# Performance work log

Measured on AMD Instinct MI355X. Metric: run time of the kernel, lower is better.

Reference implementation:

```python
import jax, jax.numpy as jnp
import numpy as np

B, C, D, H, W = 4, 256, 16, 16, 16
INTER = C // 8  # 32


def setup_inputs() -> dict:
    key = jax.random.key(0)
    ks = jax.random.split(key, 8)
    return {
        "x": jax.random.normal(ks[0], (B, C, D, H, W), dtype=jnp.float32),
        "Wq": jax.random.normal(ks[1], (INTER, C), dtype=jnp.float32) * 0.05,
        "bq": jax.random.normal(ks[2], (INTER,), dtype=jnp.float32) * 0.05,
        "Wk": jax.random.normal(ks[3], (INTER, C), dtype=jnp.float32) * 0.05,
        "bk": jax.random.normal(ks[4], (INTER,), dtype=jnp.float32) * 0.05,
        "Wv": jax.random.normal(ks[5], (C, C), dtype=jnp.float32) * 0.05,
        "bv": jax.random.normal(ks[6], (C,), dtype=jnp.float32) * 0.05,
        "gamma": jax.random.normal(ks[7], (1,), dtype=jnp.float32),
    }


def reference(x, Wq, bq, Wk, bk, Wv, bv, gamma):
    b, c, d, h, w = x.shape
    n = d * h * w
    xf = x.reshape(b, c, n)  # [B, C, N]
    # 1x1 Conv3d == pointwise channel projection
    q = jnp.einsum("oc,bcn->bon", Wq, xf) + bq[None, :, None]  # [B, inter, N]
    k = jnp.einsum("oc,bcn->bon", Wk, xf) + bk[None, :, None]  # [B, inter, N]
    v = jnp.einsum("oc,bcn->bon", Wv, xf) + bv[None, :, None]  # [B, C, N]
    scale = float(q.shape[1]) ** 0.5
    # attn[b, i, j] = <q[:, i], k[:, j]>
    attn = jax.nn.softmax(jnp.einsum("bci,bcj->bij", q, k) / scale, axis=-1)
    # out[b, c, i] = sum_j v[b, c, j] * attn[b, i, j]
    out = jnp.einsum("bcj,bij->bci", v, attn).reshape(b, c, d, h, w)
    return gamma[0] * out + x
```

## Files before the change

### kernel.cpp

```cpp
#include <hip/hip_runtime.h>

#define B_ 4
#define C_ 256
#define N_ 4096
#define INTER_ 32

typedef __attribute__((ext_vector_type(8))) short short8;
typedef __attribute__((ext_vector_type(4))) float f32x4;
typedef __attribute__((ext_vector_type(16))) float f32x16;
typedef __attribute__((ext_vector_type(4))) unsigned int u32x4;

#define TILEB 18432
#define NSTG  (8 * TILEB)

static __device__ __forceinline__ unsigned short f2bf(float f) {
    unsigned int u = __builtin_bit_cast(unsigned int, f);
    u += 0x7fff + ((u >> 16) & 1);
    return (unsigned short)(u >> 16);
}

static __device__ __forceinline__ unsigned int cvtpk(float lo, float hi) {
    unsigned int r;
    asm("v_cvt_pk_bf16_f32 %0, %1, %2" : "=v"(r) : "v"(lo), "v"(hi));
    return r;
}

static __device__ __forceinline__ void pl32swap(unsigned int& a, unsigned int& b) {
    asm("v_permlane32_swap_b32 %0, %1" : "+v"(a), "+v"(b));
}

static __device__ __forceinline__ void gload16(const void* g, void* l) {
    __builtin_amdgcn_global_load_lds(
        (const __attribute__((address_space(1))) void*)g,
        (__attribute__((address_space(3))) void*)l, 16, 0, 0);
}

__global__ __launch_bounds__(256) void prep_kernel(
    const float* __restrict__ Wq, const float* __restrict__ Wk,
    const float* __restrict__ Wv, unsigned short* __restrict__ wb)
{
    int i = blockIdx.x * 256 + threadIdx.x;
    int row = i >> 8, col = i & 255;
    float v;
    if (row < 32)      v = Wq[row * 256 + col];
    else if (row < 64) v = Wk[(row - 32) * 256 + col];
    else               v = Wv[(row - 64) * 256 + col];
    wb[i] = f2bf(v);
}

__global__ __launch_bounds__(256) void qkv_kernel(
    const float* __restrict__ x, const unsigned short* __restrict__ wb,
    const float* __restrict__ bq, const float* __restrict__ bk,
    const float* __restrict__ bv,
    unsigned short* __restrict__ qb, unsigned short* __restrict__ kfrag,
    unsigned short* __restrict__ vfrag)
{
    const int tid  = threadIdx.x;
    const int wave = tid >> 6;
    const int lane = tid & 63;
    const int l31  = lane & 31;
    const int h2   = lane >> 5;
    const int b    = blockIdx.x >> 6;
    const int n0   = (blockIdx.x & 63) * 64;

    __shared__ unsigned int xsh[64 * 129];

    {
        const float* xb = x + ((size_t)b * C_ + 64 * wave) * N_ + n0 + lane;
        unsigned int* dst = xsh + (size_t)lane * 129 + 32 * wave;
        #pragma unroll 8
        for (int s = 0; s < 32; ++s) {
            float v0 = xb[(size_t)(2 * s) * N_];
            float v1 = xb[(size_t)(2 * s + 1) * N_];
            dst[s] = (unsigned int)f2bf(v0) | ((unsigned int)f2bf(v1) << 16);
        }
    }
    __syncthreads();

    const float rs = 0.17677669529663687f;

    #pragma unroll
    for (int u = 0; u < 5; ++u) {
        const int unit = wave + 4 * u;
        const int ch = unit >> 1;
        const int ns = unit & 1;
        const int ncol = n0 + 32 * ns + l31;
        const int jt = (n0 >> 5) + ns;

        const float* bias = (ch == 0) ? bq : (ch == 1) ? bk : (bv + (ch - 2) * 32);
        f32x16 acc;
        #pragma unroll
        for (int r = 0; r < 16; ++r)
            acc[r] = bias[(r & 3) + 8 * (r >> 2) + 4 * h2];

        const unsigned short* wrow = wb + ((size_t)(ch * 32 + l31)) * 256 + 8 * h2;
        const unsigned int*   xrow = xsh + (size_t)(32 * ns + l31) * 129 + 4 * h2;

        #pragma unroll
        for (int kk = 0; kk < 16; ++kk) {
            short8 wa = *reinterpret_cast<const short8*>(wrow + 16 * kk);
            short8 xf = *reinterpret_cast<const short8*>(xrow + 8 * kk);
            acc = __builtin_amdgcn_mfma_f32_32x32x16_bf16(wa, xf, acc, 0, 0, 0);
        }

        if (ch == 0) {
            unsigned short* dst = qb + ((size_t)b * N_ + ncol) * 32;
            #pragma unroll
            for (int q = 0; q < 4; ++q) {
                unsigned int w0 = (unsigned int)f2bf(acc[4 * q] * rs)
                                | ((unsigned int)f2bf(acc[4 * q + 1] * rs) << 16);
                unsigned int w1 = (unsigned int)f2bf(acc[4 * q + 2] * rs)
                                | ((unsigned int)f2bf(acc[4 * q + 3] * rs) << 16);
                unsigned int* p = reinterpret_cast<unsigned int*>(dst + 4 * h2 + 8 * q);
                p[0] = w0; p[1] = w1;
            }
        } else if (ch == 1) {
            unsigned short* kt = kfrag + ((size_t)b * 128 + jt) * 1024;
            #pragma unroll
            for (int r = 0; r < 16; ++r) {
                const int co = (r & 3) + 8 * (r >> 2) + 4 * h2;
                const int addr = ((co >> 4) << 9) + ((l31 + 32 * ((co >> 3) & 1)) << 3)
                               + (co & 7);
                kt[addr] = f2bf(acc[r]);
            }
        } else {
            const int g = ch - 2;
            unsigned short* vt_ = vfrag + (((size_t)b * 128 + jt) * 8 + g) * 1024;
            #pragma unroll
            for (int r = 0; r < 16; ++r) {
                const int co = (r & 3) + 8 * (r >> 2) + 4 * h2;
                const int addr = ((l31 >> 4) << 9) + ((co + 32 * ((l31 >> 3) & 1)) << 3)
                               + (l31 & 7);
                vt_[addr] = f2bf(acc[r]);
            }
        }
    }
}

__global__ __launch_bounds__(512) void attn_kernel(
    const unsigned short* __restrict__ qb, const unsigned short* __restrict__ kfrag,
    const unsigned short* __restrict__ vfrag,
    const float* __restrict__ x, const float* __restrict__ gamma,
    float* __restrict__ out)
{
    const int tid  = threadIdx.x;
    const int wave = tid >> 6;
    const int lane = tid & 63;
    const int l31  = lane & 31;
    const int h2   = lane >> 5;
    const int jq   = wave >> 1;
    const int qs   = wave & 1;
    const int b    = blockIdx.y;
    const int iq   = blockIdx.x * 64 + 32 * qs;

    __shared__ char lds[NSTG];
    __shared__ float m_sh[8][32];
    __shared__ float l_sh[8][32];

    const unsigned short* vtb = vfrag + (size_t)b * 128 * 8192;
    const unsigned short* ktb = kfrag + (size_t)b * 128 * 1024;

    char* reg0 = lds + (jq * 2) * TILEB;
    char* reg1 = reg0 + TILEB;

    short8 qf0 = *reinterpret_cast<const short8*>(
        qb + ((size_t)b * N_ + iq + l31) * 32 + 8 * h2);
    short8 qf1 = *reinterpret_cast<const short8*>(
        qb + ((size_t)b * N_ + iq + l31) * 32 + 8 * h2 + 16);

    f32x16 acc[8];
    #pragma unroll
    for (int g = 0; g < 8; ++g)
        #pragma unroll
        for (int r = 0; r < 16; ++r) acc[g][r] = 0.f;

    float m_run = 0.f;
    float l_run = 0.f;
    const f32x16 z16 = {};

    {
        const char* vs = (const char*)(vtb + (size_t)(jq * 32) * 8192);
        const char* ks = (const char*)(ktb + (size_t)(jq * 32) * 1024);
        #pragma unroll
        for (int s2 = 0; s2 < 9; ++s2) {
            const int off = qs * 9216 + s2 * 1024;
            const char* g = (off < 16384) ? (vs + off) : (ks + (off - 16384));
            gload16(g + lane * 16, reg0 + off);
        }
    }
    __syncthreads();

    #pragma unroll 1
    for (int t = 0; t < 32; ++t) {
        char* cur = (t & 1) ? reg1 : reg0;
        char* nxt = (t & 1) ? reg0 : reg1;

        if (t < 31) {
            const int jtg = jq * 32 + t + 1;
            const char* vs = (const char*)(vtb + (size_t)jtg * 8192);
            const char* ks = (const char*)(ktb + (size_t)jtg * 1024);
            #pragma unroll
            for (int s2 = 0; s2 < 9; ++s2) {
                const int off = qs * 9216 + s2 * 1024;
                const char* g = (off < 16384) ? (vs + off) : (ks + (off - 16384));
                gload16(g + lane * 16, nxt + off);
            }
        }

        const char* kt_ = cur + 16384;
        short8 ka0 = *reinterpret_cast<const short8*>(kt_ + lane * 16);
        short8 ka1 = *reinterpret_cast<const short8*>(kt_ + 1024 + lane * 16);
        f32x16 s = __builtin_amdgcn_mfma_f32_32x32x16_bf16(ka0, qf0, z16, 0, 0, 0);
        s = __builtin_amdgcn_mfma_f32_32x32x16_bf16(ka1, qf1, s, 0, 0, 0);

        float a0 = fmaxf(s[0], s[8]),  a1 = fmaxf(s[1], s[9]);
        float a2 = fmaxf(s[2], s[10]), a3 = fmaxf(s[3], s[11]);
        float a4 = fmaxf(s[4], s[12]), a5 = fmaxf(s[5], s[13]);
        float a6 = fmaxf(s[6], s[14]), a7 = fmaxf(s[7], s[15]);
        a0 = fmaxf(a0, a4); a1 = fmaxf(a1, a5); a2 = fmaxf(a2, a6); a3 = fmaxf(a3, a7);
        float smax = fmaxf(fmaxf(a0, a1), fmaxf(a2, a3));

        if (__any(smax > m_run + 5.5f)) {
            float sm2 = fmaxf(smax, __shfl_xor(smax, 32));
            float mnew = fmaxf(m_run, sm2);
            float corr = __expf(m_run - mnew);
            m_run = mnew;
            l_run *= corr;
            #pragma unroll
            for (int g = 0; g < 8; ++g)
                #pragma unroll
                for (int r = 0; r < 16; ++r) acc[g][r] *= corr;
        }

        float p[16];
        float lsum = 0.f;
        #pragma unroll
        for (int r = 0; r < 16; ++r) { p[r] = __expf(s[r] - m_run); lsum += p[r]; }
        l_run += lsum;

        unsigned int X0 = cvtpk(p[0],  p[1]),  X1 = cvtpk(p[2],  p[3]);
        unsigned int Y0 = cvtpk(p[4],  p[5]),  Y1 = cvtpk(p[6],  p[7]);
        unsigned int W0 = cvtpk(p[8],  p[9]),  W1 = cvtpk(p[10], p[11]);
        unsigned int V0 = cvtpk(p[12], p[13]), V1 = cvtpk(p[14], p[15]);
        pl32swap(X0, Y0); pl32swap(X1, Y1);
        pl32swap(W0, V0); pl32swap(W1, V1);
        short8 pb0 = __builtin_bit_cast(short8, u32x4{X0, X1, Y0, Y1});
        short8 pb1 = __builtin_bit_cast(short8, u32x4{W0, W1, V0, V1});

        __builtin_amdgcn_s_setprio(1);
        #pragma unroll
        for (int g = 0; g < 8; ++g) {
            short8 va0 = *reinterpret_cast<const short8*>(cur + g * 2048 + lane * 16);
            short8 va1 = *reinterpret_cast<const short8*>(cur + g * 2048 + 1024 + lane * 16);
            acc[g] = __builtin_amdgcn_mfma_f32_32x32x16_bf16(va0, pb0, acc[g], 0, 0, 0);
            acc[g] = __builtin_amdgcn_mfma_f32_32x32x16_bf16(va1, pb1, acc[g], 0, 0, 0);
        }
        __builtin_amdgcn_s_setprio(0);

        __syncthreads();
    }

    float l_tot = l_run + __shfl_xor(l_run, 32);
    if (lane < 32) { m_sh[wave][lane] = m_run; l_sh[wave][lane] = l_tot; }
    __syncthreads();

    float M = -1e30f, L = 0.f;
    #pragma unroll
    for (int w2 = 0; w2 < 4; ++w2) M = fmaxf(M, m_sh[w2 * 2 + qs][l31]);
    #pragma unroll
    for (int w2 = 0; w2 < 4; ++w2)
        L += __expf(m_sh[w2 * 2 + qs][l31] - M) * l_sh[w2 * 2 + qs][l31];
    const float wgt = __expf(m_run - M);
    #pragma unroll
    for (int g = 0; g < 8; ++g)
        #pragma unroll
        for (int r = 0; r < 16; ++r) acc[g][r] *= wgt;

    if (jq >= 2) {
        f32x4* Dr = (f32x4*)(lds + ((jq - 2) * 2 + qs) * 32768);
        #pragma unroll
        for (int g = 0; g < 8; ++g)
            #pragma unroll
            for (int r4 = 0; r4 < 4; ++r4) {
                f32x4 tv;
                #pragma unroll
                for (int e = 0; e < 4; ++e) tv[e] = acc[g][4 * r4 + e];
                Dr[(g * 4 + r4) * 64 + lane] = tv;
            }
    }
    __syncthreads();
    if (jq < 2) {
        const f32x4* Dr = (const f32x4*)(lds + (jq * 2 + qs) * 32768);
        #pragma unroll
        for (int g = 0; g < 8; ++g)
            #pragma unroll
            for (int r4 = 0; r4 < 4; ++r4) {
                f32x4 tv = Dr[(g * 4 + r4) * 64 + lane];
                #pragma unroll
                for (int e = 0; e < 4; ++e) acc[g][4 * r4 + e] += tv[e];
            }
    }
    __syncthreads();
    if (jq == 1) {
        f32x4* Dr = (f32x4*)(lds + (2 + qs) * 32768);
        #pragma unroll
        for (int g = 0; g < 8; ++g)
            #pragma unroll
            for (int r4 = 0; r4 < 4; ++r4) {
                f32x4 tv;
                #pragma unroll
                for (int e = 0; e < 4; ++e) tv[e] = acc[g][4 * r4 + e];
                Dr[(g * 4 + r4) * 64 + lane] = tv;
            }
    }
    __syncthreads();
    if (jq == 0) {
        const f32x4* Dr = (const f32x4*)(lds + (2 + qs) * 32768);
        f32x4* Dw = (f32x4*)(lds + qs * 32768);
        #pragma unroll
        for (int g = 0; g < 8; ++g)
            #pragma unroll
            for (int r4 = 0; r4 < 4; ++r4) {
                f32x4 tv = Dr[(g * 4 + r4) * 64 + lane];
                #pragma unroll
                for (int e = 0; e < 4; ++e) tv[e] += acc[g][4 * r4 + e];
                Dw[(g * 4 + r4) * 64 + lane] = tv;
            }
    }
    __syncthreads();

    const float gma  = gamma[0];
    const float invL = 1.f / L;
    const f32x4* Ds = (const f32x4*)(lds + qs * 32768);
    const int i = iq + l31;
    #pragma unroll
    for (int gi = 0; gi < 2; ++gi) {
        const int g = jq * 2 + gi;
        #pragma unroll
        for (int r4 = 0; r4 < 4; ++r4) {
            f32x4 v = Ds[(g * 4 + r4) * 64 + lane];
            #pragma unroll
            for (int e = 0; e < 4; ++e) {
                const int c = 32 * g + e + 8 * r4 + 4 * h2;
                const size_t off = ((size_t)b * C_ + c) * N_ + i;
                out[off] = gma * v[e] * invL + x[off];
            }
        }
    }
}

extern "C" void kernel_launch(void* const* d_in, const int* in_sizes, int n_in,
                              void* d_out, int out_size, void* d_ws, size_t ws_size,
                              hipStream_t stream) {
    const float* x     = (const float*)d_in[0];
    const float* Wq    = (const float*)d_in[1];
    const float* bq    = (const float*)d_in[2];
    const float* Wk    = (const float*)d_in[3];
    const float* bk    = (const float*)d_in[4];
    const float* Wv    = (const float*)d_in[5];
    const float* bv    = (const float*)d_in[6];
    const float* gamma = (const float*)d_in[7];
    float* out = (float*)d_out;

    unsigned short* ws = (unsigned short*)d_ws;
    unsigned short* qb    = ws;
    unsigned short* kfrag = qb + (size_t)B_ * N_ * INTER_;
    unsigned short* vfrag = kfrag + (size_t)B_ * 128 * 1024;
    unsigned short* wb    = vfrag + (size_t)B_ * 128 * 8192;

    prep_kernel<<<dim3(320), 256, 0, stream>>>(Wq, Wk, Wv, wb);
    qkv_kernel<<<dim3(B_ * (N_ / 64)), 256, 0, stream>>>(
        x, wb, bq, bk, bv, qb, kfrag, vfrag);
    attn_kernel<<<dim3(N_ / 64, B_), 512, 0, stream>>>(
        qb, kfrag, vfrag, x, gamma, out);
}
```

Measured before the change: 84.60 us.

## Process two query tiles per wave, drop per-iteration block barriers, use exp2 softmax

The attention kernel now runs 4 waves per block, and each wave handles both 32-query halves of the 64-query tile. Each K/V tile loaded into LDS is therefore reused for two sets of MFMAs. Each wave streams its own K/V range into a private double buffer, which removes the per-iteration __syncthreads. The q scale is folded with log2(e) so the softmax can use exp2f, and the rescale threshold is raised. Blocks are remapped so each XCD works on one batch for L2 locality. The cost is higher register pressure from two accumulator sets, plus a serialized two-pass LDS reduction at the end.

Result: slower. 197.0 us (+132.9%).

```diff
diff --git a/kernel.cpp b/kernel.cpp
--- a/kernel.cpp
+++ b/kernel.cpp
@@ -11,7 +11,6 @@
 typedef __attribute__((ext_vector_type(4))) unsigned int u32x4;
 
 #define TILEB 18432
-#define NSTG  (8 * TILEB)
 
 static __device__ __forceinline__ unsigned short f2bf(float f) {
     unsigned int u = __builtin_bit_cast(unsigned int, f);
@@ -77,7 +76,7 @@
     }
     __syncthreads();
 
-    const float rs = 0.17677669529663687f;
+    const float rs = 0.25504183f;
 
     #pragma unroll
     for (int u = 0; u < 5; ++u) {
@@ -137,7 +136,7 @@
     }
 }
 
-__global__ __launch_bounds__(512) void attn_kernel(
+__global__ __launch_bounds__(256, 1) void attn_kernel(
     const unsigned short* __restrict__ qb, const unsigned short* __restrict__ kfrag,
     const unsigned short* __restrict__ vfrag,
     const float* __restrict__ x, const float* __restrict__ gamma,
@@ -148,202 +147,219 @@
     const int lane = tid & 63;
     const int l31  = lane & 31;
     const int h2   = lane >> 5;
-    const int jq   = wave >> 1;
-    const int qs   = wave & 1;
-    const int b    = blockIdx.y;
-    const int iq   = blockIdx.x * 64 + 32 * qs;
-
-    __shared__ char lds[NSTG];
-    __shared__ float m_sh[8][32];
-    __shared__ float l_sh[8][32];
+
+    const int bid  = blockIdx.x;
+    const int xcd  = bid & 7;
+    const int slot = bid >> 3;
+    const int b    = xcd >> 1;
+    const int ib   = slot * 2 + (xcd & 1);
+    const int i0   = ib * 64;
+
+    __shared__ char lds[4 * 2 * TILEB];
+    __shared__ float m_sh[4][2][32];
+    __shared__ float l_sh[4][2][32];
 
     const unsigned short* vtb = vfrag + (size_t)b * 128 * 8192;
     const unsigned short* ktb = kfrag + (size_t)b * 128 * 1024;
 
-    char* reg0 = lds + (jq * 2) * TILEB;
-    char* reg1 = reg0 + TILEB;
-
-    short8 qf0 = *reinterpret_cast<const short8*>(
-        qb + ((size_t)b * N_ + iq + l31) * 32 + 8 * h2);
-    short8 qf1 = *reinterpret_cast<const short8*>(
-        qb + ((size_t)b * N_ + iq + l31) * 32 + 8 * h2 + 16);
-
-    f32x16 acc[8];
+    char* buf0 = lds + wave * (2 * TILEB);
+    char* buf1 = buf0 + TILEB;
+
+#define STAGE(jtg_, dst_) do {                                                \
+        const char* vs_ = (const char*)(vtb + (size_t)(jtg_) * 8192);         \
+        _Pragma("unroll")                                                     \
+        for (int s2_ = 0; s2_ < 16; ++s2_)                                    \
+            gload16(vs_ + s2_ * 1024 + lane * 16, (dst_) + s2_ * 1024);       \
+        const char* ks_ = (const char*)(ktb + (size_t)(jtg_) * 1024);         \
+        gload16(ks_ + lane * 16, (dst_) + 16384);                             \
+        gload16(ks_ + 1024 + lane * 16, (dst_) + 17408);                      \
+    } while (0)
+
+    const unsigned short* qbase = qb + ((size_t)b * N_ + i0 + l31) * 32 + 8 * h2;
+    short8 qa0 = *reinterpret_cast<const short8*>(qbase);
+    short8 qa1 = *reinterpret_cast<const short8*>(qbase + 16);
+    short8 qb0 = *reinterpret_cast<const short8*>(qbase + 32 * 32);
+    short8 qb1 = *reinterpret_cast<const short8*>(qbase + 32 * 32 + 16);
+
+    f32x16 accA[8], accB[8];
     #pragma unroll
     for (int g = 0; g < 8; ++g)
         #pragma unroll
-        for (int r = 0; r < 16; ++r) acc[g][r] = 0.f;
-
-    float m_run = 0.f;
-    float l_run = 0.f;
+        for (int r = 0; r < 16; ++r) { accA[g][r] = 0.f; accB[g][r] = 0.f; }
+
+    float mA = 0.f, lA = 0.f, mB = 0.f, lB = 0.f;
     const f32x16 z16 = {};
 
-    {
-        const char* vs = (const char*)(vtb + (size_t)(jq * 32) * 8192);
-        const char* ks = (const char*)(ktb + (size_t)(jq * 32) * 1024);
-        #pragma unroll
-        for (int s2 = 0; s2 < 9; ++s2) {
-            const int off = qs * 9216 + s2 * 1024;
-            const char* g = (off < 16384) ? (vs + off) : (ks + (off - 16384));
-            gload16(g + lane * 16, reg0 + off);
-        }
-    }
-    __syncthreads();
+    STAGE(wave * 32, buf0);
+    asm volatile("s_waitcnt vmcnt(0)" ::: "memory");
+    __builtin_amdgcn_sched_barrier(0);
 
     #pragma unroll 1
     for (int t = 0; t < 32; ++t) {
-        char* cur = (t & 1) ? reg1 : reg0;
-        char* nxt = (t & 1) ? reg0 : reg1;
-
-        if (t < 31) {
-            const int jtg = jq * 32 + t + 1;
-            const char* vs = (const char*)(vtb + (size_t)jtg * 8192);
-            const char* ks = (const char*)(ktb + (size_t)jtg * 1024);
-            #pragma unroll
-            for (int s2 = 0; s2 < 9; ++s2) {
-                const int off = qs * 9216 + s2 * 1024;
-                const char* g = (off < 16384) ? (vs + off) : (ks + (off - 16384));
-                gload16(g + lane * 16, nxt + off);
-            }
-        }
-
-        const char* kt_ = cur + 16384;
-        short8 ka0 = *reinterpret_cast<const short8*>(kt_ + lane * 16);
-        short8 ka1 = *reinterpret_cast<const short8*>(kt_ + 1024 + lane * 16);
-        f32x16 s = __builtin_amdgcn_mfma_f32_32x32x16_bf16(ka0, qf0, z16, 0, 0, 0);
-        s = __builtin_amdgcn_mfma_f32_32x32x16_bf16(ka1, qf1, s, 0, 0, 0);
-
-        float a0 = fmaxf(s[0], s[8]),  a1 = fmaxf(s[1], s[9]);
-        float a2 = fmaxf(s[2], s[10]), a3 = fmaxf(s[3], s[11]);
-        float a4 = fmaxf(s[4], s[12]), a5 = fmaxf(s[5], s[13]);
-        float a6 = fmaxf(s[6], s[14]), a7 = fmaxf(s[7], s[15]);
-        a0 = fmaxf(a0, a4); a1 = fmaxf(a1, a5); a2 = fmaxf(a2, a6); a3 = fmaxf(a3, a7);
-        float smax = fmaxf(fmaxf(a0, a1), fmaxf(a2, a3));
-
-        if (__any(smax > m_run + 5.5f)) {
-            float sm2 = fmaxf(smax, __shfl_xor(smax, 32));
-            float mnew = fmaxf(m_run, sm2);
-            float corr = __expf(m_run - mnew);
-            m_run = mnew;
-            l_run *= corr;
-            #pragma unroll
-            for (int g = 0; g < 8; ++g)
-                #pragma unroll
-                for (int r = 0; r < 16; ++r) acc[g][r] *= corr;
-        }
-
-        float p[16];
-        float lsum = 0.f;
-        #pragma unroll
-        for (int r = 0; r < 16; ++r) { p[r] = __expf(s[r] - m_run); lsum += p[r]; }
-        l_run += lsum;
-
-        unsigned int X0 = cvtpk(p[0],  p[1]),  X1 = cvtpk(p[2],  p[3]);
-        unsigned int Y0 = cvtpk(p[4],  p[5]),  Y1 = cvtpk(p[6],  p[7]);
-        unsigned int W0 = cvtpk(p[8],  p[9]),  W1 = cvtpk(p[10], p[11]);
-        unsigned int V0 = cvtpk(p[12], p[13]), V1 = cvtpk(p[14], p[15]);
-        pl32swap(X0, Y0); pl32swap(X1, Y1);
-        pl32swap(W0, V0); pl32swap(W1, V1);
-        short8 pb0 = __builtin_bit_cast(short8, u32x4{X0, X1, Y0, Y1});
-        short8 pb1 = __builtin_bit_cast(short8, u32x4{W0, W1, V0, V1});
+        char* cur = (t & 1) ? buf1 : buf0;
+        char* nxt = (t & 1) ? buf0 : buf1;
+
+        if (t < 31) STAGE(wave * 32 + t + 1, nxt);
+
+        short8 ka0 = *reinterpret_cast<const short8*>(cur + 16384 + lane * 16);
+        short8 ka1 = *reinterpret_cast<const short8*>(cur + 17408 + lane * 16);
+        f32x16 sA = __builtin_amdgcn_mfma_f32_32x32x16_bf16(ka0, qa0, z16, 0, 0, 0);
+        sA = __builtin_amdgcn_mfma_f32_32x32x16_bf16(ka1, qa1, sA, 0, 0, 0);
+        f32x16 sB = __builtin_amdgcn_mfma_f32_32x32x16_bf16(ka0, qb0, z16, 0, 0, 0);
+        sB = __builtin_amdgcn_mfma_f32_32x32x16_bf16(ka1, qb1, sB, 0, 0, 0);
+
+        short8 pA0, pA1, pB0, pB1;
+#define SOFTMAX(s_, m_, l_, acc_, pb0_, pb1_) do {                            \
+        float a0 = fmaxf(s_[0], s_[8]),  a1 = fmaxf(s_[1], s_[9]);            \
+        float a2 = fmaxf(s_[2], s_[10]), a3 = fmaxf(s_[3], s_[11]);           \
+        float a4 = fmaxf(s_[4], s_[12]), a5 = fmaxf(s_[5], s_[13]);           \
+        float a6 = fmaxf(s_[6], s_[14]), a7 = fmaxf(s_[7], s_[15]);           \
+        a0 = fmaxf(a0, a4); a1 = fmaxf(a1, a5);                               \
+        a2 = fmaxf(a2, a6); a3 = fmaxf(a3, a7);                               \
+        float smax = fmaxf(fmaxf(a0, a1), fmaxf(a2, a3));                     \
+        if (__any(smax > m_ + 8.0f)) {                                        \
+            float sm2 = fmaxf(smax, __shfl_xor(smax, 32));                    \
+            float mnew = fmaxf(m_, sm2);                                      \
+            float corr = exp2f(m_ - mnew);                                    \
+            m_ = mnew; l_ *= corr;                                            \
+            _Pragma("unroll")                                                 \
+            for (int g_ = 0; g_ < 8; ++g_)                                    \
+                _Pragma("unroll")                                             \
+                for (int r_ = 0; r_ < 16; ++r_) acc_[g_][r_] *= corr;         \
+        }                                                                     \
+        float p_[16]; float lsum_ = 0.f;                                      \
+        _Pragma("unroll")                                                     \
+        for (int r_ = 0; r_ < 16; ++r_) {                                     \
+            p_[r_] = exp2f(s_[r_] - m_); lsum_ += p_[r_];                     \
+        }                                                                     \
+        l_ += lsum_;                                                          \
+        unsigned int X0 = cvtpk(p_[0],  p_[1]),  X1 = cvtpk(p_[2],  p_[3]);   \
+        unsigned int Y0 = cvtpk(p_[4],  p_[5]),  Y1 = cvtpk(p_[6],  p_[7]);   \
+        unsigned int W0 = cvtpk(p_[8],  p_[9]),  W1 = cvtpk(p_[10], p_[11]);  \
+        unsigned int V0 = cvtpk(p_[12], p_[13]), V1 = cvtpk(p_[14], p_[15]);  \
+        pl32swap(X0, Y0); pl32swap(X1, Y1);                                   \
+        pl32swap(W0, V0); pl32swap(W1, V1);                                   \
+        pb0_ = __builtin_bit_cast(short8, u32x4{X0, X1, Y0, Y1});             \
+        pb1_ = __builtin_bit_cast(short8, u32x4{W0, W1, V0, V1});             \
+    } while (0)
+
+        SOFTMAX(sA, mA, lA, accA, pA0, pA1);
+        SOFTMAX(sB, mB, lB, accB, pB0, pB1);
 
         __builtin_amdgcn_s_setprio(1);
         #pragma unroll
-        for (int g = 0; g < 8; ++g) {
+        for (int g = 0; g < 4; ++g) {
             short8 va0 = *reinterpret_cast<const short8*>(cur + g * 2048 + lane * 16);
             short8 va1 = *reinterpret_cast<const short8*>(cur + g * 2048 + 1024 + lane * 16);
-            acc[g] = __builtin_amdgcn_mfma_f32_32x32x16_bf16(va0, pb0, acc[g], 0, 0, 0);
-            acc[g] = __builtin_amdgcn_mfma_f32_32x32x16_bf16(va1, pb1, acc[g], 0, 0, 0);
+            accA[g] = __builtin_amdgcn_mfma_f32_32x32x16_bf16(va0, pA0, accA[g], 0, 0, 0);
+            accA[g] = __builtin_amdgcn_mfma_f32_32x32x16_bf16(va1, pA1, accA[g], 0, 0, 0);
+            accB[g] = __builtin_amdgcn_mfma_f32_32x32x16_bf16(va0, pB0, accB[g], 0, 0, 0);
+            accB[g] = __builtin_amdgcn_mfma_f32_32x32x16_bf16(va1, pB1, accB[g], 0, 0, 0);
+        }
+        __builtin_amdgcn_sched_barrier(0);
+        #pragma unroll
+        for (int g = 4; g < 8; ++g) {
+            short8 va0 = *reinterpret_cast<const short8*>(cur + g * 2048 + lane * 16);
+            short8 va1 = *reinterpret_cast<const short8*>(cur + g * 2048 + 1024 + lane * 16);
+            accA[g] = __builtin_amdgcn_mfma_f32_32x32x16_bf16(va0, pA0, accA[g], 0, 0, 0);
+            accA[g] = __builtin_amdgcn_mfma_f32_32x32x16_bf16(va1, pA1, accA[g], 0, 0, 0);
+            accB[g] = __builtin_amdgcn_mfma_f32_32x32x16_bf16(va0, pB0, accB[g], 0, 0, 0);
+            accB[g] = __builtin_amdgcn_mfma_f32_32x32x16_bf16(va1, pB1, accB[g], 0, 0, 0);
         }
         __builtin_amdgcn_s_setprio(0);
 
-        __syncthreads();
-    }
-
-    float l_tot = l_run + __shfl_xor(l_run, 32);
-    if (lane < 32) { m_sh[wave][lane] = m_run; l_sh[wave][lane] = l_tot; }
-    __syncthreads();
-
-    float M = -1e30f, L = 0.f;
-    #pragma unroll
-    for (int w2 = 0; w2 < 4; ++w2) M = fmaxf(M, m_sh[w2 * 2 + qs][l31]);
-    #pragma unroll
-    for (int w2 = 0; w2 < 4; ++w2)
-        L += __expf(m_sh[w2 * 2 + qs][l31] - M) * l_sh[w2 * 2 + qs][l31];
-    const float wgt = __expf(m_run - M);
+        asm volatile("s_waitcnt vmcnt(0)" ::: "memory");
+        __builtin_amdgcn_sched_barrier(0);
+    }
+#undef STAGE
+#undef SOFTMAX
+
+    float ltA = lA + __shfl_xor(lA, 32);
+    float ltB = lB + __shfl_xor(lB, 32);
+    if (lane < 32) {
+        m_sh[wave][0][lane] = mA; l_sh[wave][0][lane] = ltA;
+        m_sh[wave][1][lane] = mB; l_sh[wave][1][lane] = ltB;
+    }
+    __syncthreads();
+
+    float MA = -1e30f, MB = -1e30f, LA = 0.f, LB = 0.f;
+    #pragma unroll
+    for (int w = 0; w < 4; ++w) {
+        MA = fmaxf(MA, m_sh[w][0][l31]);
+        MB = fmaxf(MB, m_sh[w][1][l31]);
+    }
+    #pragma unroll
+    for (int w = 0; w < 4; ++w) {
+        LA += exp2f(m_sh[w][0][l31] - MA) * l_sh[w][0][l31];
+        LB += exp2f(m_sh[w][1][l31] - MB) * l_sh[w][1][l31];
+    }
+    const float wgtA = exp2f(mA - MA);
+    const float wgtB = exp2f(mB - MB);
     #pragma unroll
     for (int g = 0; g < 8; ++g)
         #pragma unroll
-        for (int r = 0; r < 16; ++r) acc[g][r] *= wgt;
-
-    if (jq >= 2) {
-        f32x4* Dr = (f32x4*)(lds + ((jq - 2) * 2 + qs) * 32768);
-        #pragma unroll
-        for (int g = 0; g < 8; ++g)
-            #pragma unroll
-            for (int r4 = 0; r4 < 4; ++r4) {
-                f32x4 tv;
-                #pragma unroll
-                for (int e = 0; e < 4; ++e) tv[e] = acc[g][4 * r4 + e];
-                Dr[(g * 4 + r4) * 64 + lane] = tv;
-            }
-    }
-    __syncthreads();
-    if (jq < 2) {
-        const f32x4* Dr = (const f32x4*)(lds + (jq * 2 + qs) * 32768);
-        #pragma unroll
-        for (int g = 0; g < 8; ++g)
-            #pragma unroll
-            for (int r4 = 0; r4 < 4; ++r4) {
-                f32x4 tv = Dr[(g * 4 + r4) * 64 + lane];
-                #pragma unroll
-                for (int e = 0; e < 4; ++e) acc[g][4 * r4 + e] += tv[e];
-            }
-    }
-    __syncthreads();
-    if (jq == 1) {
-        f32x4* Dr = (f32x4*)(lds + (2 + qs) * 32768);
-        #pragma unroll
-        for (int g = 0; g < 8; ++g)
-            #pragma unroll
-            for (int r4 = 0; r4 < 4; ++r4) {
-                f32x4 tv;
-                #pragma unroll
-                for (int e = 0; e < 4; ++e) tv[e] = acc[g][4 * r4 + e];
-                Dr[(g * 4 + r4) * 64 + lane] = tv;
-            }
-    }
-    __syncthreads();
-    if (jq == 0) {
-        const f32x4* Dr = (const f32x4*)(lds + (2 + qs) * 32768);
-        f32x4* Dw = (f32x4*)(lds + qs * 32768);
-        #pragma unroll
-        for (int g = 0; g < 8; ++g)
-            #pragma unroll
-            for (int r4 = 0; r4 < 4; ++r4) {
-                f32x4 tv = Dr[(g * 4 + r4) * 64 + lane];
-                #pragma unroll
-                for (int e = 0; e < 4; ++e) tv[e] += acc[g][4 * r4 + e];
-                Dw[(g * 4 + r4) * 64 + lane] = tv;
-            }
-    }
-    __syncthreads();
+        for (int r = 0; r < 16; ++r) { accA[g][r] *= wgtA; accB[g][r] *= wgtB; }
 
     const float gma  = gamma[0];
-    const float invL = 1.f / L;
-    const f32x4* Ds = (const f32x4*)(lds + qs * 32768);
-    const int i = iq + l31;
+    const float invLA = 1.f / LA;
+    const float invLB = 1.f / LB;
+    f32x4* D = reinterpret_cast<f32x4*>(lds);
+
+    #pragma unroll
+    for (int g = 0; g < 8; ++g)
+        #pragma unroll
+        for (int r4 = 0; r4 < 4; ++r4) {
+            f32x4 tv;
+            #pragma unroll
+            for (int e = 0; e < 4; ++e) tv[e] = accA[g][4 * r4 + e];
+            D[((wave * 8 + g) * 4 + r4) * 64 + lane] = tv;
+        }
+    __syncthreads();
     #pragma unroll
     for (int gi = 0; gi < 2; ++gi) {
-        const int g = jq * 2 + gi;
+        const int g = wave * 2 + gi;
         #pragma unroll
         for (int r4 = 0; r4 < 4; ++r4) {
-            f32x4 v = Ds[(g * 4 + r4) * 64 + lane];
+            f32x4 s0 = D[((0 * 8 + g) * 4 + r4) * 64 + lane];
+            f32x4 s1 = D[((1 * 8 + g) * 4 + r4) * 64 + lane];
+            f32x4 s2 = D[((2 * 8 + g) * 4 + r4) * 64 + lane];
+            f32x4 s3 = D[((3 * 8 + g) * 4 + r4) * 64 + lane];
             #pragma unroll
             for (int e = 0; e < 4; ++e) {
+                const float v = s0[e] + s1[e] + s2[e] + s3[e];
                 const int c = 32 * g + e + 8 * r4 + 4 * h2;
-                const size_t off = ((size_t)b * C_ + c) * N_ + i;
-                out[off] = gma * v[e] * invL + x[off];
+                const size_t off = ((size_t)b * C_ + c) * N_ + i0 + l31;
+                out[off] = gma * v * invLA + x[off];
+            }
+        }
+    }
+    __syncthreads();
+
+    #pragma unroll
+    for (int g = 0; g < 8; ++g)
+        #pragma unroll
+        for (int r4 = 0; r4 < 4; ++r4) {
+            f32x4 tv;
+            #pragma unroll
+            for (int e = 0; e < 4; ++e) tv[e] = accB[g][4 * r4 + e];
+            D[((wave * 8 + g) * 4 + r4) * 64 + lane] = tv;
+        }
+    __syncthreads();
+    #pragma unroll
+    for (int gi = 0; gi < 2; ++gi) {
+        const int g = wave * 2 + gi;
+        #pragma unroll
+        for (int r4 = 0; r4 < 4; ++r4) {
+            f32x4 s0 = D[((0 * 8 + g) * 4 + r4) * 64 + lane];
+            f32x4 s1 = D[((1 * 8 + g) * 4 + r4) * 64 + lane];
+            f32x4 s2 = D[((2 * 8 + g) * 4 + r4) * 64 + lane];
+            f32x4 s3 = D[((3 * 8 + g) * 4 + r4) * 64 + lane];
+            #pragma unroll
+            for (int e = 0; e < 4; ++e) {
+                const float v = s0[e] + s1[e] + s2[e] + s3[e];
+                const int c = 32 * g + e + 8 * r4 + 4 * h2;
+                const size_t off = ((size_t)b * C_ + c) * N_ + i0 + 32 + l31;
+                out[off] = gma * v * invLB + x[off];
             }
         }
     }
@@ -371,6 +387,6 @@
     prep_kernel<<<dim3(320), 256, 0, stream>>>(Wq, Wk, Wv, wb);
     qkv_kernel<<<dim3(B_ * (N_ / 64)), 256, 0, stream>>>(
         x, wb, bq, bk, bv, qb, kfrag, vfrag);
-    attn_kernel<<<dim3(N_ / 64, B_), 512, 0, stream>>>(
+    attn_kernel<<<dim3(256), 256, 0, stream>>>(
         qb, kfrag, vfrag, x, gamma, out);
 }
```
